# Optimization experiments

Hardware: AMD Instinct MI355X
Metric: run time of the kernel (lower is better)

## Reference

```python
import jax, jax.numpy as jnp
import numpy as np
from jax import lax

B, T, D, H = 4, 2048, 1024, 8
DK = D // H        # head qk dim (expand_k=1.0) = 128
DV = 2 * D // H    # head v dim (expand_v=2.0) = 256
C = 64             # retention chunk size


def setup_inputs() -> dict:
    key = jax.random.key(0)
    ks = jax.random.split(key, 7)
    s = 0.02
    return {
        "x": jax.random.normal(ks[0], (B, T, D), jnp.float32),
        "Wq": jax.random.normal(ks[1], (D, H * DK), jnp.float32) * s,
        "Wk": jax.random.normal(ks[2], (D, H * DK), jnp.float32) * s,
        "Wv": jax.random.normal(ks[3], (D, H * DV), jnp.float32) * s,
        "Wg": jax.random.normal(ks[4], (D, H * DV), jnp.float32) * s,
        "Wo": jax.random.normal(ks[5], (H * DV, D), jnp.float32) * s,
        "norm_w": jnp.ones((DV,), jnp.float32),
    }


def _rope(x):
    # x: [B,T,H,DK]; GPT-NeoX style (non-interleaved) rotary, base 10000
    half = DK // 2
    inv = 1.0 / (10000.0 ** (jnp.arange(0, DK, 2, dtype=jnp.float32) / DK))
    f = jnp.arange(T, dtype=jnp.float32)[:, None] * inv[None, :]  # [T, half]
    cos = jnp.cos(f)[None, :, None, :]
    sin = jnp.sin(f)[None, :, None, :]
    x1, x2 = x[..., :half], x[..., half:]
    return jnp.concatenate([x1 * cos - x2 * sin, x2 * cos + x1 * sin], axis=-1)


def _retention(q, k, v):
    # chunked decay-gated linear attention (RetNet retention)
    # q,k: [B,T,H,DK], v: [B,T,H,DV]; recurrence S_t = g*S_{t-1} + k_t^T v_t, o_t = q_t S_t
    N = T // C
    gamma = 1.0 - 2.0 ** (-5.0 - jnp.arange(H, dtype=jnp.float32))  # [H] per-head decay
    i = jnp.arange(C, dtype=jnp.float32)
    expo = i[:, None] - i[None, :]                                   # [C,C]
    M = jnp.where(expo >= 0, gamma[:, None, None] ** expo[None], 0.0)  # [H,C,C] intra-chunk decay mask
    dec_q = gamma[:, None] ** (i + 1.0)        # [H,C] decay of state seen by q_i
    dec_k = gamma[:, None] ** (C - 1.0 - i)    # [H,C] decay of k_j into end-of-chunk state
    gC = gamma ** C

    def to_chunks(t):
        return t.reshape(B, N, C, H, -1).transpose(1, 0, 3, 2, 4)  # [N,B,H,C,d]

    qs, kcs, vcs = to_chunks(q), to_chunks(k), to_chunks(v)

    def step(S, inp):
        qc, kc, vc = inp  # [B,H,C,DK],[B,H,C,DK],[B,H,C,DV]
        attn = jnp.einsum('bhid,bhjd->bhij', qc, kc) * M[None]
        o_intra = jnp.einsum('bhij,bhje->bhie', attn, vc)
        o_inter = jnp.einsum('bhid,bhde->bhie', qc, S) * dec_q[None, :, :, None]
        kv = jnp.einsum('bhjd,bhje->bhde', kc * dec_k[None, :, :, None], vc)
        S_new = gC[None, :, None, None] * S + kv
        return S_new, o_intra + o_inter

    S0 = jnp.zeros((B, H, DK, DV), q.dtype)
    _, os_ = lax.scan(step, S0, (qs, kcs, vcs))  # os_: [N,B,H,C,DV]
    return os_.transpose(1, 0, 3, 2, 4).reshape(B, T, H, DV)


def reference(x, Wq, Wk, Wv, Wg, Wo, norm_w):
    q = (x @ Wq).reshape(B, T, H, DK)
    k = (x @ Wk).reshape(B, T, H, DK)
    v = (x @ Wv).reshape(B, T, H, DV)
    g = (x @ Wg).reshape(B, T, H, DV)
    q, k = _rope(q), _rope(k)
    q = q * (DK ** -0.5)
    o = _retention(q, k, v)
    # fused per-head RMSNorm + swish output gate (FusedRMSNormSwishGate)
    rms = jnp.sqrt(jnp.mean(o * o, axis=-1, keepdims=True) + 1e-5)
    o = (o / rms) * norm_w
    o = o * g * jax.nn.sigmoid(g)
    return o.reshape(B, T, H * DV) @ Wo
```

## Files before the change

kernel.cpp:

```cpp
#include <hip/hip_runtime.h>
#include <hip/hip_bf16.h>
#include <cstdint>
#include <cstddef>

using f32x4 = __attribute__((ext_vector_type(4))) float;
using s16x8 = __attribute__((ext_vector_type(8))) short;
using s16x4 = __attribute__((ext_vector_type(4))) short;

#define DEVINL __device__ __forceinline__

static constexpr int T_LEN  = 2048;
static constexpr int MROWS  = 8192;
static constexpr int NCHUNK = 32;

DEVINL float bf2f(short s){
  unsigned u = ((unsigned)(unsigned short)s) << 16;
  return __builtin_bit_cast(float, u);
}
DEVINL short f2bf(float f){
  unsigned u = __builtin_bit_cast(unsigned, f);
  u = (u + 0x7fffu + ((u >> 16) & 1u)) >> 16;
  return (short)(unsigned short)u;
}

#define GLOAD16(gp, lp) \
  __builtin_amdgcn_global_load_lds((__attribute__((address_space(1))) void*)(gp), \
                                   (__attribute__((address_space(3))) void*)(lp), 16, 0, 0)

#define MFMA16(a, b, c) __builtin_amdgcn_mfma_f32_16x16x32_bf16((a), (b), (c), 0, 0, 0)

__global__ __launch_bounds__(256) void cvt_f32_bf16(const float* __restrict__ in,
                                                    short* __restrict__ out, int n4){
  int i = blockIdx.x * 256 + threadIdx.x;
  if (i >= n4) return;
  float4 v = ((const float4*)in)[i];
  short4 o;
  o.x = f2bf(v.x); o.y = f2bf(v.y); o.z = f2bf(v.z); o.w = f2bf(v.w);
  ((short4*)out)[i] = o;
}

__global__ __launch_bounds__(256) void tr_w(const float* __restrict__ in,
                                            short* __restrict__ out, int R, int C){
  __shared__ float tile[32][33];
  int c0 = blockIdx.x * 32, r0 = blockIdx.y * 32;
  int tx = threadIdx.x, ty = threadIdx.y;
  #pragma unroll
  for (int i = 0; i < 4; ++i){
    int r = ty + i * 8;
    tile[r][tx] = in[(size_t)(r0 + r) * C + c0 + tx];
  }
  __syncthreads();
  #pragma unroll
  for (int i = 0; i < 4; ++i){
    int c = ty + i * 8;
    out[(size_t)(c0 + c) * R + r0 + tx] = f2bf(tile[tx][c]);
  }
}

__global__ __launch_bounds__(256) void tr_k_decay(const short* __restrict__ in,
                                                  short* __restrict__ out){
  __shared__ float tile[32][33];
  int c0 = blockIdx.x * 32, r0 = blockIdx.y * 32;
  int tx = threadIdx.x, ty = threadIdx.y;
  #pragma unroll
  for (int i = 0; i < 4; ++i){
    int r = ty + i * 8;
    tile[r][tx] = bf2f(in[(size_t)(r0 + r) * 1024 + c0 + tx]);
  }
  __syncthreads();
  #pragma unroll
  for (int i = 0; i < 4; ++i){
    int c  = c0 + ty + i * 8;
    int h  = c >> 7;
    float lg = log2f(1.0f - exp2f(-(float)(5 + h)));
    int srow = r0 + tx;
    int j = srow & 63;
    float dec = exp2f((float)(63 - j) * lg);
    out[(size_t)c * MROWS + srow] = f2bf(tile[tx][ty + i * 8] * dec);
  }
}

__global__ __launch_bounds__(256) void rope_table(float* __restrict__ tab){
  int i = blockIdx.x * 256 + threadIdx.x;
  int t = i >> 6, d = i & 63;
  float inv = exp2f(-(float)d * (13.287712379549449f / 64.0f));
  float f = (float)t * inv;
  float s, c;
  sincosf(f, &s, &c);
  tab[2 * i]     = c;
  tab[2 * i + 1] = s;
}

__global__ __launch_bounds__(256) void rope_inplace(short* __restrict__ qk,
                                                    const float* __restrict__ tab,
                                                    float scale, int bake){
  int idx = blockIdx.x * 256 + threadIdx.x;
  int bt  = idx >> 9, rem = idx & 511;
  int h   = rem >> 6, d = rem & 63;
  int t   = bt & (T_LEN - 1);
  float2 cs = ((const float2*)tab)[t * 64 + d];
  float mult = scale;
  if (bake){
    float lg = log2f(1.0f - exp2f(-(float)(5 + h)));
    mult *= exp2f((float)((t & 63) + 1) * lg);
  }
  size_t base = (size_t)bt * 1024 + h * 128 + d;
  float x1 = bf2f(qk[base]), x2 = bf2f(qk[base + 64]);
  qk[base]      = f2bf((x1 * cs.x - x2 * cs.y) * mult);
  qk[base + 64] = f2bf((x2 * cs.x + x1 * cs.y) * mult);
}

template<int MODE>
__global__ __launch_bounds__(256) void gemm_bt(const short* __restrict__ A,
                                               const short* __restrict__ Bt,
                                               void* __restrict__ out, int K, int N){
  __shared__ alignas(16) short As[128 * 64];
  __shared__ alignas(16) short Bs[128 * 64];
  const int tid = threadIdx.x, wave = tid >> 6, lane = tid & 63;
  const int m0 = blockIdx.x * 128, n0 = blockIdx.y * 128;
  const int wm = (wave & 1) * 64, wn = (wave >> 1) * 64;
  f32x4 acc[4][4] = {};
  const int srow = wave * 8 + (lane >> 3);
  const int sc   = lane & 7;
  const int kT = K >> 6;
  for (int kt = 0; kt < kT; ++kt){
    const int k0 = kt << 6;
    #pragma unroll
    for (int c = 0; c < 4; ++c){
      int row = c * 32 + srow;
      int gc  = sc ^ (row & 7);
      GLOAD16(A  + (size_t)(m0 + row) * K + k0 + gc * 8, &As[c * 2048 + wave * 512]);
      GLOAD16(Bt + (size_t)(n0 + row) * K + k0 + gc * 8, &Bs[c * 2048 + wave * 512]);
    }
    __syncthreads();
    #pragma unroll
    for (int ks = 0; ks < 2; ++ks){
      s16x8 af[4], bfr[4];
      #pragma unroll
      for (int mf = 0; mf < 4; ++mf){
        int row = wm + mf * 16 + (lane & 15);
        int ch  = (ks * 4 + (lane >> 4)) ^ (row & 7);
        af[mf] = *(const s16x8*)&As[row * 64 + ch * 8];
      }
      #pragma unroll
      for (int nf = 0; nf < 4; ++nf){
        int row = wn + nf * 16 + (lane & 15);
        int ch  = (ks * 4 + (lane >> 4)) ^ (row & 7);
        bfr[nf] = *(const s16x8*)&Bs[row * 64 + ch * 8];
      }
      #pragma unroll
      for (int mf = 0; mf < 4; ++mf)
        #pragma unroll
        for (int nf = 0; nf < 4; ++nf)
          acc[mf][nf] = MFMA16(af[mf], bfr[nf], acc[mf][nf]);
    }
    __syncthreads();
  }
  #pragma unroll
  for (int mf = 0; mf < 4; ++mf){
    #pragma unroll
    for (int nf = 0; nf < 4; ++nf){
      int col   = n0 + wn + nf * 16 + (lane & 15);
      int rbase = m0 + wm + mf * 16 + 4 * (lane >> 4);
      f32x4 v = acc[mf][nf];
      if (MODE == 0){
        short* o = (short*)out;
        #pragma unroll
        for (int r = 0; r < 4; ++r) o[(size_t)(rbase + r) * N + col] = f2bf(v[r]);
      } else if (MODE == 1){
        short* o = (short*)out;
        s16x4 pk; pk[0] = f2bf(v[0]); pk[1] = f2bf(v[1]); pk[2] = f2bf(v[2]); pk[3] = f2bf(v[3]);
        *(s16x4*)&o[(size_t)col * MROWS + rbase] = pk;
      } else {
        float* o = (float*)out;
        #pragma unroll
        for (int r = 0; r < 4; ++r) o[(size_t)(rbase + r) * N + col] = v[r];
      }
    }
  }
}

__global__ __launch_bounds__(256) void ret_scan(const short* __restrict__ kT,
                                                const short* __restrict__ vT,
                                                short* __restrict__ ST){
  __shared__ alignas(16) short kbuf[3][4096];
  __shared__ alignas(16) short vbuf[3][4096];
  const int tid = threadIdx.x, wave = tid >> 6, lane = tid & 63;
  const int db = blockIdx.x & 1, eb = blockIdx.x >> 1;
  const int h = blockIdx.y, b = blockIdx.z;
  const int d0 = db * 64, e0 = eb * 64;
  const float lg = log2f(1.0f - exp2f(-(float)(5 + h)));
  const float gC = exp2f(64.0f * lg);
  f32x4 Sacc[4] = {};
  const int srow = wave * 8 + (lane >> 3);
  const int sc   = lane & 7;

  auto STAGE = [&](int n, int buf){
    size_t rowbase = (size_t)(b * T_LEN + n * 64);
    #pragma unroll
    for (int c = 0; c < 2; ++c){
      int r = c * 32 + srow;
      int gc = sc ^ (r & 7);
      GLOAD16(kT + (size_t)(h * 128 + d0 + r) * MROWS + rowbase + gc * 8,
              &kbuf[buf][c * 2048 + wave * 512]);
    }
    #pragma unroll
    for (int c = 0; c < 2; ++c){
      int r = c * 32 + srow;
      int gc = sc ^ (r & 7);
      GLOAD16(vT + (size_t)(h * 256 + e0 + r) * MROWS + rowbase + gc * 8,
              &vbuf[buf][c * 2048 + wave * 512]);
    }
  };

  STAGE(0, 0);
  STAGE(1, 1);
  for (int n = 0; n < NCHUNK; ++n){
    const int buf = n % 3;
    if (n + 2 < NCHUNK) STAGE(n + 2, (n + 2) % 3);
    if (n > 0){
      size_t stb = (((size_t)n * 4 + b) * 8 + h) * 32768;
      int dbase = d0 + 16 * wave + 4 * (lane >> 4);
      #pragma unroll
      for (int nf = 0; nf < 4; ++nf){
        int e = e0 + nf * 16 + (lane & 15);
        s16x4 pk;
        #pragma unroll
        for (int r = 0; r < 4; ++r) pk[r] = f2bf(Sacc[nf][r]);
        *(s16x4*)&ST[stb + (size_t)e * 128 + dbase] = pk;
      }
    }
    if (n == 0)       asm volatile("s_waitcnt vmcnt(8)"  ::: "memory");
    else if (n < 30)  asm volatile("s_waitcnt vmcnt(12)" ::: "memory");
    else if (n == 30) asm volatile("s_waitcnt vmcnt(8)"  ::: "memory");
    else              asm volatile("s_waitcnt vmcnt(4)"  ::: "memory");
    __builtin_amdgcn_s_barrier();
    __builtin_amdgcn_sched_barrier(0);
    #pragma unroll
    for (int nf = 0; nf < 4; ++nf)
      #pragma unroll
      for (int r = 0; r < 4; ++r) Sacc[nf][r] *= gC;
    #pragma unroll
    for (int ks = 0; ks < 2; ++ks){
      int d = 16 * wave + (lane & 15);
      int chA = (ks * 4 + (lane >> 4)) ^ (d & 7);
      s16x8 af = *(const s16x8*)&kbuf[buf][d * 64 + chA * 8];
      #pragma unroll
      for (int nf = 0; nf < 4; ++nf){
        int e = nf * 16 + (lane & 15);
        int chB = (ks * 4 + (lane >> 4)) ^ (e & 7);
        s16x8 bv = *(const s16x8*)&vbuf[buf][e * 64 + chB * 8];
        Sacc[nf] = MFMA16(af, bv, Sacc[nf]);
      }
    }
    __builtin_amdgcn_s_barrier();
    __builtin_amdgcn_sched_barrier(0);
  }
}

__global__ __launch_bounds__(256, 2) void ret_fused(const short* __restrict__ q,
                                                    const short* __restrict__ k,
                                                    const short* __restrict__ vT,
                                                    const short* __restrict__ ST,
                                                    const short* __restrict__ g,
                                                    const float* __restrict__ nw,
                                                    short* __restrict__ y){
  __shared__ alignas(16) short GS[16384];
  __shared__ alignas(16) float SS[256];
  __shared__ alignas(16) short XS[16896];
  short* PS = XS;
  short* YT = XS;
  const int tid = threadIdx.x, wave = tid >> 6, lane = tid & 63;
  const int l15 = lane & 15, lhi = lane >> 4;
  const int n = blockIdx.x, h = blockIdx.y, b = blockIdx.z;
  const size_t rowbase = (size_t)(b * T_LEN + n * 64);
  {
    int row = wave * 2 + (lane >> 5), sc32 = lane & 31;
    #pragma unroll
    for (int c = 0; c < 8; ++c){
      int r = c * 8 + row;
      GLOAD16(g + (rowbase + r) * 2048 + h * 256 + sc32 * 8, &GS[c * 2048 + wave * 512]);
    }
  }
  s16x8 Qf[4][4];
  #pragma unroll
  for (int rf = 0; rf < 4; ++rf)
    #pragma unroll
    for (int ks = 0; ks < 4; ++ks)
      Qf[rf][ks] = *(const s16x8*)&q[(rowbase + rf * 16 + l15) * 1024 + h * 128 + ks * 32 + lhi * 8];
  s16x8 Kf[4];
  #pragma unroll
  for (int ks = 0; ks < 4; ++ks)
    Kf[ks] = *(const s16x8*)&k[(rowbase + wave * 16 + l15) * 1024 + h * 128 + ks * 32 + lhi * 8];
  f32x4 accP[4] = {};
  #pragma unroll
  for (int ks = 0; ks < 4; ++ks)
    #pragma unroll
    for (int nf = 0; nf < 4; ++nf)
      accP[nf] = MFMA16(Kf[ks], Qf[nf][ks], accP[nf]);
  const float lg = log2f(1.0f - exp2f(-(float)(5 + h)));
  {
    int jb = wave * 16 + 4 * lhi;
    float dj[4];
    #pragma unroll
    for (int r = 0; r < 4; ++r) dj[r] = exp2f(-(float)(jb + r + 1) * lg);
    #pragma unroll
    for (int nf = 0; nf < 4; ++nf){
      int i = nf * 16 + l15;
      s16x4 pk;
      #pragma unroll
      for (int r = 0; r < 4; ++r)
        pk[r] = f2bf((i >= jb + r) ? accP[nf][r] * dj[r] : 0.0f);
      *(s16x4*)&PS[i * 72 + jb] = pk;
    }
  }
  f32x4 acc[4][4] = {};
  if (n){
    size_t stb = (((size_t)n * 4 + b) * 8 + h) * 32768;
    #pragma unroll
    for (int ks = 0; ks < 4; ++ks){
      s16x8 Sf[4];
      #pragma unroll
      for (int nf = 0; nf < 4; ++nf){
        int e = wave * 64 + nf * 16 + l15;
        Sf[nf] = *(const s16x8*)&ST[stb + (size_t)e * 128 + ks * 32 + lhi * 8];
      }
      #pragma unroll
      for (int mf = 0; mf < 4; ++mf)
        #pragma unroll
        for (int nf = 0; nf < 4; ++nf)
          acc[mf][nf] = MFMA16(Qf[mf][ks], Sf[nf], acc[mf][nf]);
    }
  }
  s16x8 Vf[2][4];
  #pragma unroll
  for (int ks2 = 0; ks2 < 2; ++ks2)
    #pragma unroll
    for (int nf = 0; nf < 4; ++nf){
      int e = wave * 64 + nf * 16 + l15;
      Vf[ks2][nf] = *(const s16x8*)&vT[(size_t)(h * 256 + e) * MROWS + rowbase + ks2 * 32 + lhi * 8];
    }
  __syncthreads();
  #pragma unroll
  for (int ks2 = 0; ks2 < 2; ++ks2){
    s16x8 Pf[4];
    #pragma unroll
    for (int mf = 0; mf < 4; ++mf)
      Pf[mf] = *(const s16x8*)&PS[(mf * 16 + l15) * 72 + ks2 * 32 + lhi * 8];
    #pragma unroll
    for (int mf = 0; mf < 4; ++mf)
      #pragma unroll
      for (int nf = 0; nf < 4; ++nf)
        acc[mf][nf] = MFMA16(Pf[mf], Vf[ks2][nf], acc[mf][nf]);
  }
  float ssp[4][4];
  #pragma unroll
  for (int mf = 0; mf < 4; ++mf)
    #pragma unroll
    for (int r = 0; r < 4; ++r){
      float s = 0.f;
      #pragma unroll
      for (int nf = 0; nf < 4; ++nf) s += acc[mf][nf][r] * acc[mf][nf][r];
      #pragma unroll
      for (int off = 8; off >= 1; off >>= 1) s += __shfl_xor(s, off, 64);
      ssp[mf][r] = s;
    }
  if (l15 == 0){
    #pragma unroll
    for (int mf = 0; mf < 4; ++mf)
      #pragma unroll
      for (int r = 0; r < 4; ++r){
        int row = mf * 16 + 4 * lhi + r;
        SS[row * 4 + wave] = ssp[mf][r];
      }
  }
  __syncthreads();
  #pragma unroll
  for (int mf = 0; mf < 4; ++mf){
    float rr[4];
    #pragma unroll
    for (int r = 0; r < 4; ++r){
      int row = mf * 16 + 4 * lhi + r;
      f32x4 s4 = *(const f32x4*)&SS[row * 4];
      float tot = s4[0] + s4[1] + s4[2] + s4[3];
      rr[r] = __builtin_amdgcn_rsqf(tot * (1.0f / 256.0f) + 1e-5f);
    }
    #pragma unroll
    for (int nf = 0; nf < 4; ++nf){
      int e = wave * 64 + nf * 16 + l15;
      float nwe = nw[e];
      #pragma unroll
      for (int r = 0; r < 4; ++r){
        int row = mf * 16 + 4 * lhi + r;
        float gf = bf2f(GS[row * 256 + e]);
        float sig = __builtin_amdgcn_rcpf(1.0f + exp2f(gf * -1.4426950408889634f));
        YT[row * 264 + e] = f2bf(acc[mf][nf][r] * rr[r] * nwe * gf * sig);
      }
    }
  }
  __syncthreads();
  #pragma unroll
  for (int it = 0; it < 8; ++it){
    int flat = it * 2048 + tid * 8;
    int row = flat >> 8, e = flat & 255;
    s16x8 v = *(const s16x8*)&YT[row * 264 + e];
    *(s16x8*)&y[(rowbase + row) * 2048 + h * 256 + e] = v;
  }
}

extern "C" void kernel_launch(void* const* d_in, const int* in_sizes, int n_in,
                              void* d_out, int out_size, void* d_ws, size_t ws_size,
                              hipStream_t stream){
  const float* x  = (const float*)d_in[0];
  const float* Wq = (const float*)d_in[1];
  const float* Wk = (const float*)d_in[2];
  const float* Wv = (const float*)d_in[3];
  const float* Wg = (const float*)d_in[4];
  const float* Wo = (const float*)d_in[5];
  const float* nw = (const float*)d_in[6];
  float* out = (float*)d_out;

  char* w = (char*)d_ws;
  short* xb  = (short*)w;               w += (size_t)8192 * 1024 * 2;
  short* WT  = (short*)w;               w += (size_t)6144 * 1024 * 2;
  short* kTt = (short*)w;               w += (size_t)1024 * 8192 * 2;
  short* qb  = (short*)w;               w += (size_t)8192 * 1024 * 2;
  short* kb  = (short*)w;               w += (size_t)8192 * 1024 * 2;
  short* vT  = (short*)w;               w += (size_t)2048 * 8192 * 2;
  short* gb  = (short*)w;               w += (size_t)8192 * 2048 * 2;
  short* STb = (short*)w;               w += (size_t)32 * 4 * 8 * 32768 * 2;
  short* WoT = (short*)w;               w += (size_t)1024 * 2048 * 2;
  short* yb  = (short*)d_ws;
  float* tab = (float*)STb;

  cvt_f32_bf16<<<8192, 256, 0, stream>>>(x, xb, 8192 * 1024 / 4);
  dim3 tb(32, 8);
  tr_w<<<dim3(32, 32), tb, 0, stream>>>(Wq, WT,                       1024, 1024);
  tr_w<<<dim3(32, 32), tb, 0, stream>>>(Wk, WT + (size_t)1024 * 1024, 1024, 1024);
  tr_w<<<dim3(64, 32), tb, 0, stream>>>(Wv, WT + (size_t)2048 * 1024, 1024, 2048);
  tr_w<<<dim3(64, 32), tb, 0, stream>>>(Wg, WT + (size_t)4096 * 1024, 1024, 2048);
  tr_w<<<dim3(32, 64), tb, 0, stream>>>(Wo, WoT,                      2048, 1024);
  rope_table<<<512, 256, 0, stream>>>(tab);

  gemm_bt<0><<<dim3(64,  8), 256, 0, stream>>>(xb, WT,                       qb, 1024, 1024);
  gemm_bt<0><<<dim3(64,  8), 256, 0, stream>>>(xb, WT + (size_t)1024 * 1024, kb, 1024, 1024);
  gemm_bt<1><<<dim3(64, 16), 256, 0, stream>>>(xb, WT + (size_t)2048 * 1024, vT, 1024, 2048);
  gemm_bt<0><<<dim3(64, 16), 256, 0, stream>>>(xb, WT + (size_t)4096 * 1024, gb, 1024, 2048);

  rope_inplace<<<16384, 256, 0, stream>>>(qb, tab, 0.08838834764831845f, 1);
  rope_inplace<<<16384, 256, 0, stream>>>(kb, tab, 1.0f, 0);
  tr_k_decay<<<dim3(32, 256), tb, 0, stream>>>(kb, kTt);

  ret_scan <<<dim3(8, 8, 4),  256, 0, stream>>>(kTt, vT, STb);
  ret_fused<<<dim3(32, 8, 4), 256, 0, stream>>>(qb, kb, vT, STb, gb, nw, yb);
  gemm_bt<2><<<dim3(64, 8), 256, 0, stream>>>(yb, WoT, out, 2048, 1024);
}
```

Baseline: 323.1 us.

## Replace projection GEMMs with one fused 256x256 pipelined GEMM kernel

Replaces the 128x128 single-buffered gemm_bt with a 256x256-tile, 512-thread kernel that double-buffers A and B in LDS and staggers global loads across the four compute quarters. It uses explicit waitcnt, barriers and setprio to overlap loads with MFMA work. The four input projections (q, k, v-transposed, g) become a single launch over the concatenated weight matrix, with per-tile output routing and an L2-friendly block swizzle. The output projection uses the same kernel. Larger tiles raise data reuse but give only 128 blocks for the Wo GEMM, which may underfill the GPU, and the hand-tuned waitcnt counts are fragile.

```diff
diff --git a/kernel.cpp b/kernel.cpp
--- a/kernel.cpp
+++ b/kernel.cpp
@@ -110,71 +110,145 @@
   qk[base + 64] = f2bf((x2 * cs.x + x1 * cs.y) * mult);
 }
 
+DEVINL void stage_half(const short* __restrict__ src, int ldk, int t, int half,
+                       short* lbase, int wave, int lane){
+  const int sr = lane >> 3;
+  const int gc = ((lane & 7) ^ sr) * 8;
+  const size_t k0 = (size_t)t * 64;
+  #pragma unroll
+  for (int c = 0; c < 2; ++c){
+    int r0 = half * 128 + c * 64;
+    GLOAD16(src + (size_t)(r0 + wave * 8 + sr) * ldk + k0 + gc,
+            lbase + (r0 + wave * 8) * 64);
+  }
+}
+
+DEVINL s16x8 frag64(const short* buf, int row, int ks, int lhi){
+  int ch = (ks * 4 + lhi) ^ (row & 7);
+  return *(const s16x8*)&buf[row * 64 + ch * 8];
+}
+
 template<int MODE>
-__global__ __launch_bounds__(256) void gemm_bt(const short* __restrict__ A,
-                                               const short* __restrict__ Bt,
-                                               void* __restrict__ out, int K, int N){
-  __shared__ alignas(16) short As[128 * 64];
-  __shared__ alignas(16) short Bs[128 * 64];
+__global__ __launch_bounds__(512, 2) void gemm256(const short* __restrict__ A,
+                                                  const short* __restrict__ Bt,
+                                                  void* __restrict__ o0, void* __restrict__ o1,
+                                                  void* __restrict__ o2, void* __restrict__ o3,
+                                                  int K, int nt){
+  __shared__ alignas(16) short LBUF[65536];
   const int tid = threadIdx.x, wave = tid >> 6, lane = tid & 63;
-  const int m0 = blockIdx.x * 128, n0 = blockIdx.y * 128;
-  const int wm = (wave & 1) * 64, wn = (wave >> 1) * 64;
-  f32x4 acc[4][4] = {};
-  const int srow = wave * 8 + (lane >> 3);
-  const int sc   = lane & 7;
-  const int kT = K >> 6;
-  for (int kt = 0; kt < kT; ++kt){
-    const int k0 = kt << 6;
-    #pragma unroll
-    for (int c = 0; c < 4; ++c){
-      int row = c * 32 + srow;
-      int gc  = sc ^ (row & 7);
-      GLOAD16(A  + (size_t)(m0 + row) * K + k0 + gc * 8, &As[c * 2048 + wave * 512]);
-      GLOAD16(Bt + (size_t)(n0 + row) * K + k0 + gc * 8, &Bs[c * 2048 + wave * 512]);
-    }
-    __syncthreads();
-    #pragma unroll
-    for (int ks = 0; ks < 2; ++ks){
-      s16x8 af[4], bfr[4];
-      #pragma unroll
-      for (int mf = 0; mf < 4; ++mf){
-        int row = wm + mf * 16 + (lane & 15);
-        int ch  = (ks * 4 + (lane >> 4)) ^ (row & 7);
-        af[mf] = *(const s16x8*)&As[row * 64 + ch * 8];
-      }
+  const int l15 = lane & 15, lhi = lane >> 4;
+  const int wm = (wave >> 2) * 128, wn = (wave & 3) * 64;
+  const int cpx = gridDim.x >> 3;
+  const int swz = (blockIdx.x & 7) * cpx + (blockIdx.x >> 3);
+  const int m0 = (swz & 31) * 256, n0 = (swz >> 5) * 256;
+  const short* Ag = A + (size_t)m0 * K;
+  const short* Bg = Bt + (size_t)n0 * K;
+  f32x4 acc[8][4] = {};
+  stage_half(Ag, K, 0, 0, LBUF,                 wave, lane);
+  stage_half(Ag, K, 0, 1, LBUF,                 wave, lane);
+  stage_half(Bg, K, 0, 0, LBUF + 32768,         wave, lane);
+  stage_half(Bg, K, 0, 1, LBUF + 32768,         wave, lane);
+  stage_half(Bg, K, 1, 0, LBUF + 32768 + 16384, wave, lane);
+  stage_half(Bg, K, 1, 1, LBUF + 32768 + 16384, wave, lane);
+  asm volatile("s_waitcnt vmcnt(4)" ::: "memory");
+  __builtin_amdgcn_sched_barrier(0);
+  __builtin_amdgcn_s_barrier();
+  for (int t = 0; t < nt; ++t){
+    short* Ab = LBUF + (t & 1) * 16384;
+    short* Bb = LBUF + 32768 + (t & 1) * 16384;
+    s16x8 bfr[2][4];
+    #pragma unroll
+    for (int q = 0; q < 4; ++q){
+      if (q == 0){
+        #pragma unroll
+        for (int ks = 0; ks < 2; ++ks)
+          #pragma unroll
+          for (int nf = 0; nf < 4; ++nf)
+            bfr[ks][nf] = frag64(Bb, wn + nf * 16 + l15, ks, lhi);
+      }
+      s16x8 af[2][2];
+      #pragma unroll
+      for (int i = 0; i < 2; ++i)
+        #pragma unroll
+        for (int ks = 0; ks < 2; ++ks)
+          af[i][ks] = frag64(Ab, wm + (2 * q + i) * 16 + l15, ks, lhi);
+      if (q == 0 && t + 1 < nt) stage_half(Ag, K, t + 1, 0, LBUF + ((t + 1) & 1) * 16384, wave, lane);
+      if (q == 1 && t + 1 < nt) stage_half(Ag, K, t + 1, 1, LBUF + ((t + 1) & 1) * 16384, wave, lane);
+      if (q == 2 && t + 2 < nt) stage_half(Bg, K, t + 2, 0, LBUF + 32768 + (t & 1) * 16384, wave, lane);
+      if (q == 3 && t + 2 < nt) stage_half(Bg, K, t + 2, 1, LBUF + 32768 + (t & 1) * 16384, wave, lane);
+      __builtin_amdgcn_sched_barrier(0);
+      __builtin_amdgcn_s_barrier();
+      asm volatile("s_waitcnt lgkmcnt(0)" ::: "memory");
+      __builtin_amdgcn_sched_barrier(0);
+      __builtin_amdgcn_s_setprio(1);
+      #pragma unroll
+      for (int i = 0; i < 2; ++i)
+        #pragma unroll
+        for (int nf = 0; nf < 4; ++nf)
+          #pragma unroll
+          for (int ks = 0; ks < 2; ++ks)
+            acc[2 * q + i][nf] = MFMA16(af[i][ks], bfr[ks][nf], acc[2 * q + i][nf]);
+      __builtin_amdgcn_s_setprio(0);
+      if (q == 3){
+        if (t < nt - 2)       asm volatile("s_waitcnt vmcnt(4)" ::: "memory");
+        else if (t == nt - 2) asm volatile("s_waitcnt vmcnt(0)" ::: "memory");
+        __builtin_amdgcn_sched_barrier(0);
+      }
+      __builtin_amdgcn_s_barrier();
+    }
+  }
+  if (MODE == 2){
+    float* dst = (float*)o0;
+    #pragma unroll
+    for (int mf = 0; mf < 8; ++mf){
+      int rb = m0 + wm + mf * 16 + 4 * lhi;
       #pragma unroll
       for (int nf = 0; nf < 4; ++nf){
-        int row = wn + nf * 16 + (lane & 15);
-        int ch  = (ks * 4 + (lane >> 4)) ^ (row & 7);
-        bfr[nf] = *(const s16x8*)&Bs[row * 64 + ch * 8];
-      }
-      #pragma unroll
-      for (int mf = 0; mf < 4; ++mf)
-        #pragma unroll
-        for (int nf = 0; nf < 4; ++nf)
-          acc[mf][nf] = MFMA16(af[mf], bfr[nf], acc[mf][nf]);
-    }
-    __syncthreads();
-  }
-  #pragma unroll
-  for (int mf = 0; mf < 4; ++mf){
-    #pragma unroll
-    for (int nf = 0; nf < 4; ++nf){
-      int col   = n0 + wn + nf * 16 + (lane & 15);
-      int rbase = m0 + wm + mf * 16 + 4 * (lane >> 4);
-      f32x4 v = acc[mf][nf];
-      if (MODE == 0){
-        short* o = (short*)out;
-        #pragma unroll
-        for (int r = 0; r < 4; ++r) o[(size_t)(rbase + r) * N + col] = f2bf(v[r]);
-      } else if (MODE == 1){
-        short* o = (short*)out;
-        s16x4 pk; pk[0] = f2bf(v[0]); pk[1] = f2bf(v[1]); pk[2] = f2bf(v[2]); pk[3] = f2bf(v[3]);
-        *(s16x4*)&o[(size_t)col * MROWS + rbase] = pk;
-      } else {
-        float* o = (float*)out;
-        #pragma unroll
-        for (int r = 0; r < 4; ++r) o[(size_t)(rbase + r) * N + col] = v[r];
+        int col = n0 + wn + nf * 16 + l15;
+        #pragma unroll
+        for (int r = 0; r < 4; ++r) dst[(size_t)(rb + r) * 1024 + col] = acc[mf][nf][r];
+      }
+    }
+  } else {
+    if (n0 < 2048){
+      short* dst = (short*)(n0 < 1024 ? o0 : o1);
+      int cb = (n0 & 1023) + wn;
+      #pragma unroll
+      for (int mf = 0; mf < 8; ++mf){
+        int rb = m0 + wm + mf * 16 + 4 * lhi;
+        #pragma unroll
+        for (int nf = 0; nf < 4; ++nf){
+          int col = cb + nf * 16 + l15;
+          #pragma unroll
+          for (int r = 0; r < 4; ++r) dst[(size_t)(rb + r) * 1024 + col] = f2bf(acc[mf][nf][r]);
+        }
+      }
+    } else if (n0 < 4096){
+      short* dst = (short*)o2;
+      #pragma unroll
+      for (int mf = 0; mf < 8; ++mf){
+        int rb = m0 + wm + mf * 16 + 4 * lhi;
+        #pragma unroll
+        for (int nf = 0; nf < 4; ++nf){
+          int e = (n0 - 2048) + wn + nf * 16 + l15;
+          s16x4 pk;
+          #pragma unroll
+          for (int r = 0; r < 4; ++r) pk[r] = f2bf(acc[mf][nf][r]);
+          *(s16x4*)&dst[(size_t)e * MROWS + rb] = pk;
+        }
+      }
+    } else {
+      short* dst = (short*)o3;
+      int cb = (n0 - 4096) + wn;
+      #pragma unroll
+      for (int mf = 0; mf < 8; ++mf){
+        int rb = m0 + wm + mf * 16 + 4 * lhi;
+        #pragma unroll
+        for (int nf = 0; nf < 4; ++nf){
+          int col = cb + nf * 16 + l15;
+          #pragma unroll
+          for (int r = 0; r < 4; ++r) dst[(size_t)(rb + r) * 2048 + col] = f2bf(acc[mf][nf][r]);
+        }
       }
     }
   }
@@ -442,10 +516,7 @@
   tr_w<<<dim3(32, 64), tb, 0, stream>>>(Wo, WoT,                      2048, 1024);
   rope_table<<<512, 256, 0, stream>>>(tab);
 
-  gemm_bt<0><<<dim3(64,  8), 256, 0, stream>>>(xb, WT,                       qb, 1024, 1024);
-  gemm_bt<0><<<dim3(64,  8), 256, 0, stream>>>(xb, WT + (size_t)1024 * 1024, kb, 1024, 1024);
-  gemm_bt<1><<<dim3(64, 16), 256, 0, stream>>>(xb, WT + (size_t)2048 * 1024, vT, 1024, 2048);
-  gemm_bt<0><<<dim3(64, 16), 256, 0, stream>>>(xb, WT + (size_t)4096 * 1024, gb, 1024, 2048);
+  gemm256<3><<<768, 512, 0, stream>>>(xb, WT, qb, kb, vT, gb, 1024, 16);
 
   rope_inplace<<<16384, 256, 0, stream>>>(qb, tab, 0.08838834764831845f, 1);
   rope_inplace<<<16384, 256, 0, stream>>>(kb, tab, 1.0f, 0);
@@ -453,5 +524,6 @@
 
   ret_scan <<<dim3(8, 8, 4),  256, 0, stream>>>(kTt, vT, STb);
   ret_fused<<<dim3(32, 8, 4), 256, 0, stream>>>(qb, kb, vT, STb, gb, nw, yb);
-  gemm_bt<2><<<dim3(64, 8), 256, 0, stream>>>(yb, WoT, out, 2048, 1024);
-}
+
+  gemm256<2><<<128, 512, 0, stream>>>(yb, WoT, out, nullptr, nullptr, nullptr, 2048, 32);
+}
```

Result: faster. 307.1 us (-5.0%).
